# Performance work log

Hardware: AMD Instinct MI355X
Metric: run time of the kernel (lower is better)

Reference implementation:

```python
import jax, jax.numpy as jnp
import numpy as np

B, T, D, H = 4, 4096, 1280, 5120  # batch, tokens (64x64 SAM grid), embedding_dim, mlp_dim


def setup_inputs() -> dict:
    key = jax.random.key(0)
    k = jax.random.split(key, 5)
    # int8 quantized activations and weights (symmetric, per-tensor)
    x = jax.random.randint(k[0], (B, T, D), -128, 128, dtype=jnp.int8)
    w1 = jax.random.randint(k[1], (H, D), -128, 128, dtype=jnp.int8)  # lin1.weight [out,in]
    b1 = jax.random.normal(k[2], (H,), jnp.float32) * 0.02            # fp32 bias
    w2 = jax.random.randint(k[3], (D, H), -128, 128, dtype=jnp.int8)  # lin2.weight [out,in]
    b2 = jax.random.normal(k[4], (D,), jnp.float32) * 0.02
    a1 = jnp.float32(0.05 * 0.01)   # input_scale * w1_scale (dequant alpha of lin1)
    s_req = jnp.float32(0.08)       # lin2_input_scale (requant scale after GELU)
    a2 = jnp.float32(0.08 * 0.01)   # lin2_input_scale * w2_scale (dequant alpha of lin2)
    return dict(x=x, w1=w1, b1=b1, w2=w2, b2=b2, a1=a1, s_req=s_req, a2=a2)


def reference(x, w1, b1, w2, b2, a1, s_req, a2):
    acc1 = jnp.einsum('btd,hd->bth', x.astype(jnp.int32), w1.astype(jnp.int32))
    h = acc1.astype(jnp.float32) * a1 + b1              # [B,T,H] fp32
    # exact (erf) GELU, then requantize to int8 for lin2's input
    g = jax.nn.gelu(h, approximate=False)
    q = jnp.clip(jnp.round(g / s_req), -128, 127).astype(jnp.int8)
    acc2 = jnp.einsum('bth,dh->btd', q.astype(jnp.int32), w2.astype(jnp.int32))
    return acc2.astype(jnp.float32) * a2 + b2           # [B,T,D] fp32
```

## Files before the change

kernel.cpp:

```cpp
#include <hip/hip_runtime.h>
#include <stdint.h>
#include <math.h>

typedef __attribute__((ext_vector_type(4))) int i32x4;
typedef __attribute__((ext_vector_type(4))) float f32x4;

constexpr int D_DIM = 1280;
constexpr int H_DIM = 5120;

__device__ __forceinline__ void gload_lds16(const void* g, void* l) {
  __builtin_amdgcn_global_load_lds(
      (const __attribute__((address_space(1))) void*)g,
      (__attribute__((address_space(3))) void*)l,
      16, 0, 0);
}

__device__ __forceinline__ float gelu_fast(float h) {
  const float x = h * 0.70710678118f;
  const float ax = fabsf(x);
  const float t = __frcp_rn(__builtin_fmaf(0.3275911f, ax, 1.0f));
  float p = __builtin_fmaf(1.061405429f, t, -1.453152027f);
  p = __builtin_fmaf(p, t, 1.421413741f);
  p = __builtin_fmaf(p, t, -0.284496736f);
  p = __builtin_fmaf(p, t, 0.254829592f);
  p *= t;
  const float e = __expf(-x * x);
  const float erf_ax = __builtin_fmaf(-p, e, 1.0f);
  const float erf_x = copysignf(erf_ax, x);
  return 0.5f * h * (1.0f + erf_x);
}

__global__ void __launch_bounds__(256) k_packw(const int* __restrict__ s1,
                                               const int* __restrict__ s2,
                                               int8_t* __restrict__ out,
                                               long wn) {
  long i = ((long)blockIdx.x * 256 + threadIdx.x) * 16;
  const int* p = (i < wn) ? (s1 + i) : (s2 + (i - wn));
  i32x4 a = *(const i32x4*)(p);
  i32x4 b = *(const i32x4*)(p + 4);
  i32x4 c = *(const i32x4*)(p + 8);
  i32x4 d = *(const i32x4*)(p + 12);
  i32x4 r;
  r.x = (a.x & 255) | ((a.y & 255) << 8) | ((a.z & 255) << 16) | (a.w << 24);
  r.y = (b.x & 255) | ((b.y & 255) << 8) | ((b.z & 255) << 16) | (b.w << 24);
  r.z = (c.x & 255) | ((c.y & 255) << 8) | ((c.z & 255) << 16) | (c.w << 24);
  r.w = (d.x & 255) | ((d.y & 255) << 8) | ((d.z & 255) << 16) | (d.w << 24);
  *(i32x4*)(out + i) = r;
}

__global__ void __launch_bounds__(256) k_pack(const int* __restrict__ in,
                                              int8_t* __restrict__ out,
                                              long n) {
  long i = ((long)blockIdx.x * 256 + threadIdx.x) * 16;
  if (i >= n) return;
  const int* p = in + i;
  i32x4 a = *(const i32x4*)(p);
  i32x4 b = *(const i32x4*)(p + 4);
  i32x4 c = *(const i32x4*)(p + 8);
  i32x4 d = *(const i32x4*)(p + 12);
  i32x4 r;
  r.x = (a.x & 255) | ((a.y & 255) << 8) | ((a.z & 255) << 16) | (a.w << 24);
  r.y = (b.x & 255) | ((b.y & 255) << 8) | ((b.z & 255) << 16) | (b.w << 24);
  r.z = (c.x & 255) | ((c.y & 255) << 8) | ((c.z & 255) << 16) | (c.w << 24);
  r.w = (d.x & 255) | ((d.y & 255) << 8) | ((d.z & 255) << 16) | (d.w << 24);
  *(i32x4*)(out + i) = r;
}

template <int KDIM, int NDIM, bool GELU>
__global__ void __launch_bounds__(256, 2)
k_gemm(const int8_t* __restrict__ A, const int8_t* __restrict__ B,
       const float* __restrict__ bias, const float* __restrict__ ps1,
       const float* __restrict__ ps2, void* __restrict__ Cout, int Mtiles) {
  constexpr int BM = 128, BN = 128, BKB = 128;
  constexpr int NT = KDIM / BKB;
  constexpr int BNC = NDIM / BN;
  constexpr int G = BNC * 4;

  __shared__ __align__(16) int8_t As[2][BM * BKB];
  __shared__ __align__(16) int8_t Bs[2][BN * BKB];

  const int nwg = Mtiles * BNC;
  int bm, bn;
  {
    const int bid = blockIdx.x;
    const int q = nwg >> 3, r = nwg & 7, x = bid & 7, l = bid >> 3;
    const int swz = (x < r ? x * (q + 1) : r * (q + 1) + (x - r) * q) + l;
    if ((Mtiles & 3) == 0) {
      const int g = swz / G, rr = swz % G;
      bn = rr >> 2;
      bm = g * 4 + (rr & 3);
    } else {
      bn = swz % BNC;
      bm = swz / BNC;
    }
  }

  const int tid = threadIdx.x;
  const int lane = tid & 63, wid = tid >> 6;
  const int wr = wid >> 1, wc = wid & 1;

  const int srow = tid >> 3;
  const int soff = (((tid & 7) ^ (srow & 7)) << 4);
  const int8_t* Ath = A + (size_t)(bm * BM + srow) * KDIM + soff;
  const int8_t* Bth = B + (size_t)(bn * BN + srow) * KDIM + soff;
  const int dT = tid * 16;

  auto STAGE = [&](int buf, int t) {
    const int8_t* ga = Ath + t * BKB;
    const int8_t* gb = Bth + t * BKB;
#pragma unroll
    for (int p = 0; p < 4; ++p)
      gload_lds16(ga + (size_t)(p * 32) * KDIM, &As[buf][dT + p * 4096]);
#pragma unroll
    for (int p = 0; p < 4; ++p)
      gload_lds16(gb + (size_t)(p * 32) * KDIM, &Bs[buf][dT + p * 4096]);
  };

  const int r0 = lane & 15, kq = (lane >> 4) << 4;
  const int fsw = (r0 & 7) << 4;
  const int kof0 = kq ^ fsw;
  const int kof1 = (64 + kq) ^ fsw;
  const int rowA0 = (wr * 64 + r0) * BKB;
  const int rowB0 = (wc * 64 + r0) * BKB;

  i32x4 acc[4][4] = {};

  auto COMPUTE = [&](int buf) {
    const int8_t* Ac = As[buf];
    const int8_t* Bc = Bs[buf];
#pragma unroll
    for (int j = 0; j < 2; ++j) {
      const int kof = j ? kof1 : kof0;
      i32x4 af[4], bf[4];
#pragma unroll
      for (int m = 0; m < 4; ++m) af[m] = *(const i32x4*)(Ac + rowA0 + m * 2048 + kof);
#pragma unroll
      for (int n = 0; n < 4; ++n) bf[n] = *(const i32x4*)(Bc + rowB0 + n * 2048 + kof);
      if constexpr (GELU) {
#pragma unroll
        for (int n = 0; n < 4; ++n)
#pragma unroll
          for (int m = 0; m < 4; ++m)
            acc[n][m] =
                __builtin_amdgcn_mfma_i32_16x16x64_i8(bf[n], af[m], acc[n][m], 0, 0, 0);
      } else {
#pragma unroll
        for (int m = 0; m < 4; ++m)
#pragma unroll
          for (int n = 0; n < 4; ++n)
            acc[m][n] =
                __builtin_amdgcn_mfma_i32_16x16x64_i8(af[m], bf[n], acc[m][n], 0, 0, 0);
      }
    }
  };

  STAGE(0, 0);
  __syncthreads();
#pragma unroll 1
  for (int t = 0; t < NT; ++t) {
    const int cur = t & 1;
    if (t + 1 < NT) STAGE(cur ^ 1, t + 1);
    COMPUTE(cur);
    __syncthreads();
  }

  const int hq = lane >> 4;
  if constexpr (GELU) {
    const float s1 = *ps1;
    const float rs = 1.0f / (*ps2);
    int8_t* Q = (int8_t*)Cout;
    const int hb0 = bn * BN + wc * 64 + hq * 4;
    const int tok0 = bm * BM + wr * 64 + r0;
#pragma unroll
    for (int n = 0; n < 4; ++n) {
      const int hb = hb0 + n * 16;
      const f32x4 bv = *(const f32x4*)(bias + hb);
#pragma unroll
      for (int m = 0; m < 4; ++m) {
        const int tok = tok0 + m * 16;
        uint32_t pk = 0;
#pragma unroll
        for (int r = 0; r < 4; ++r) {
          const float h = __builtin_fmaf((float)acc[n][m][r], s1, bv[r]);
          float qf = rintf(gelu_fast(h) * rs);
          qf = fminf(127.0f, fmaxf(-128.0f, qf));
          pk |= ((uint32_t)((int)qf & 255)) << (r * 8);
        }
        *(uint32_t*)(Q + (size_t)tok * NDIM + hb) = pk;
      }
    }
  } else {
    const float s1 = *ps1;
    float* O = (float*)Cout;
    const int rowb = bm * BM + wr * 64 + hq * 4;
    const int colb = bn * BN + wc * 64 + r0;
#pragma unroll
    for (int n = 0; n < 4; ++n) {
      const int col = colb + n * 16;
      const float bv = bias[col];
#pragma unroll
      for (int m = 0; m < 4; ++m) {
#pragma unroll
        for (int r = 0; r < 4; ++r) {
          const int row = rowb + m * 16 + r;
          O[(size_t)row * NDIM + col] = __builtin_fmaf((float)acc[m][n][r], s1, bv);
        }
      }
    }
  }
}

extern "C" void kernel_launch(void* const* d_in, const int* in_sizes, int n_in,
                              void* d_out, int out_size, void* d_ws, size_t ws_size,
                              hipStream_t stream) {
  (void)in_sizes; (void)n_in; (void)out_size;
  const int*   x32  = (const int*)d_in[0];
  const int*   w132 = (const int*)d_in[1];
  const float* b1   = (const float*)d_in[2];
  const int*   w232 = (const int*)d_in[3];
  const float* b2   = (const float*)d_in[4];
  const float* a1   = (const float*)d_in[5];
  const float* sreq = (const float*)d_in[6];
  const float* a2   = (const float*)d_in[7];
  float* out = (float*)d_out;

  const int M = 4 * 4096;
  const size_t WN = (size_t)H_DIM * D_DIM;
  constexpr int BM = 128, BN = 128;

  int8_t* w1p  = (int8_t*)d_ws;
  int8_t* w2p  = w1p + WN;
  int8_t* base = w2p + WN;

  size_t avail = ws_size > 2 * WN ? ws_size - 2 * WN : 0;
  size_t rows = avail / (size_t)(D_DIM + H_DIM);
  int Mc = (int)((rows / BM) * BM);
  if (Mc > M) Mc = M;
  if (Mc < BM) Mc = BM;

  k_packw<<<(int)(2 * WN / 4096), 256, 0, stream>>>(w132, w232, w1p, (long)WN);

  for (int m0 = 0; m0 < M; m0 += Mc) {
    const int mc = (M - m0 < Mc) ? (M - m0) : Mc;
    int8_t* xp = base;
    int8_t* q  = base + (size_t)Mc * D_DIM;
    const size_t nx = (size_t)mc * D_DIM;
    const int mt = mc / BM;
    k_pack<<<(int)(nx / 4096), 256, 0, stream>>>(x32 + (size_t)m0 * D_DIM, xp, (long)nx);
    k_gemm<D_DIM, H_DIM, true><<<mt * (H_DIM / BN), 256, 0, stream>>>(
        xp, w1p, b1, a1, sreq, q, mt);
    k_gemm<H_DIM, D_DIM, false><<<mt * (D_DIM / BN), 256, 0, stream>>>(
        q, w2p, b2, a2, nullptr, out + (size_t)m0 * D_DIM, mt);
  }
}
```

Measured before the change: 333.4 us.

## Switch int8 GEMMs to 32x32x32 MFMA with LDS-staged coalesced GELU output

Replaces the 16x16x64 int8 MFMA tiling with 32x32x32 MFMA instructions, a 2x2 grid of 32x32 accumulators per wave, and fewer LDS fragment loads per k-step. The main loop is unrolled by two with a fixed double-buffer layout in one flat shared array and precomputed fragment pointers. The GELU epilogue now writes packed int8 results into swizzled LDS and then does coalesced 16-byte global stores instead of scattered 4-byte stores. This adds an extra barrier and LDS round trip in the epilogue, and the unrolled loop assumes an even number of k-tiles.

```diff
diff --git a/kernel.cpp b/kernel.cpp
--- a/kernel.cpp
+++ b/kernel.cpp
@@ -3,6 +3,7 @@
 #include <math.h>
 
 typedef __attribute__((ext_vector_type(4))) int i32x4;
+typedef __attribute__((ext_vector_type(16))) int i32x16;
 typedef __attribute__((ext_vector_type(4))) float f32x4;
 
 constexpr int D_DIM = 1280;
@@ -76,8 +77,7 @@
   constexpr int BNC = NDIM / BN;
   constexpr int G = BNC * 4;
 
-  __shared__ __align__(16) int8_t As[2][BM * BKB];
-  __shared__ __align__(16) int8_t Bs[2][BN * BKB];
+  __shared__ __align__(16) int8_t smem[4 * 16384];
 
   const int nwg = Mtiles * BNC;
   int bm, bn;
@@ -105,106 +105,121 @@
   const int8_t* Bth = B + (size_t)(bn * BN + srow) * KDIM + soff;
   const int dT = tid * 16;
 
-  auto STAGE = [&](int buf, int t) {
-    const int8_t* ga = Ath + t * BKB;
-    const int8_t* gb = Bth + t * BKB;
+  auto STAGE = [&](int boff, const int8_t* ga, const int8_t* gb) {
 #pragma unroll
     for (int p = 0; p < 4; ++p)
-      gload_lds16(ga + (size_t)(p * 32) * KDIM, &As[buf][dT + p * 4096]);
+      gload_lds16(ga + (size_t)(p * 32) * KDIM, smem + boff + dT + p * 4096);
 #pragma unroll
     for (int p = 0; p < 4; ++p)
-      gload_lds16(gb + (size_t)(p * 32) * KDIM, &Bs[buf][dT + p * 4096]);
+      gload_lds16(gb + (size_t)(p * 32) * KDIM,
+                  smem + 32768 + boff + dT + p * 4096);
   };
 
-  const int r0 = lane & 15, kq = (lane >> 4) << 4;
-  const int fsw = (r0 & 7) << 4;
-  const int kof0 = kq ^ fsw;
-  const int kof1 = (64 + kq) ^ fsw;
-  const int rowA0 = (wr * 64 + r0) * BKB;
-  const int rowB0 = (wc * 64 + r0) * BKB;
-
-  i32x4 acc[4][4] = {};
-
-  auto COMPUTE = [&](int buf) {
-    const int8_t* Ac = As[buf];
-    const int8_t* Bc = Bs[buf];
-#pragma unroll
-    for (int j = 0; j < 2; ++j) {
-      const int kof = j ? kof1 : kof0;
-      i32x4 af[4], bf[4];
-#pragma unroll
-      for (int m = 0; m < 4; ++m) af[m] = *(const i32x4*)(Ac + rowA0 + m * 2048 + kof);
-#pragma unroll
-      for (int n = 0; n < 4; ++n) bf[n] = *(const i32x4*)(Bc + rowB0 + n * 2048 + kof);
+  const int r32 = lane & 31, hi5 = lane >> 5;
+  const int fsw = (lane & 7) << 4;
+  const int kq = hi5 << 4;
+  const int8_t* aP[4];
+  const int8_t* bP[4];
+#pragma unroll
+  for (int ks = 0; ks < 4; ++ks) {
+    const int koff = (ks * 32 + kq) ^ fsw;
+    aP[ks] = smem + (wr * 64 + r32) * BKB + koff;
+    bP[ks] = smem + 32768 + (wc * 64 + r32) * BKB + koff;
+  }
+
+  i32x16 acc[2][2] = {};
+
+  auto COMPUTE = [&](int boff) {
+#pragma unroll
+    for (int ks = 0; ks < 4; ++ks) {
+      i32x4 a0 = *(const i32x4*)(aP[ks] + boff);
+      i32x4 a1 = *(const i32x4*)(aP[ks] + boff + 4096);
+      i32x4 b0 = *(const i32x4*)(bP[ks] + boff);
+      i32x4 b1 = *(const i32x4*)(bP[ks] + boff + 4096);
       if constexpr (GELU) {
-#pragma unroll
-        for (int n = 0; n < 4; ++n)
-#pragma unroll
-          for (int m = 0; m < 4; ++m)
-            acc[n][m] =
-                __builtin_amdgcn_mfma_i32_16x16x64_i8(bf[n], af[m], acc[n][m], 0, 0, 0);
+        acc[0][0] = __builtin_amdgcn_mfma_i32_32x32x32_i8(b0, a0, acc[0][0], 0, 0, 0);
+        acc[0][1] = __builtin_amdgcn_mfma_i32_32x32x32_i8(b0, a1, acc[0][1], 0, 0, 0);
+        acc[1][0] = __builtin_amdgcn_mfma_i32_32x32x32_i8(b1, a0, acc[1][0], 0, 0, 0);
+        acc[1][1] = __builtin_amdgcn_mfma_i32_32x32x32_i8(b1, a1, acc[1][1], 0, 0, 0);
       } else {
-#pragma unroll
-        for (int m = 0; m < 4; ++m)
-#pragma unroll
-          for (int n = 0; n < 4; ++n)
-            acc[m][n] =
-                __builtin_amdgcn_mfma_i32_16x16x64_i8(af[m], bf[n], acc[m][n], 0, 0, 0);
+        acc[0][0] = __builtin_amdgcn_mfma_i32_32x32x32_i8(a0, b0, acc[0][0], 0, 0, 0);
+        acc[0][1] = __builtin_amdgcn_mfma_i32_32x32x32_i8(a0, b1, acc[0][1], 0, 0, 0);
+        acc[1][0] = __builtin_amdgcn_mfma_i32_32x32x32_i8(a1, b0, acc[1][0], 0, 0, 0);
+        acc[1][1] = __builtin_amdgcn_mfma_i32_32x32x32_i8(a1, b1, acc[1][1], 0, 0, 0);
       }
     }
   };
 
-  STAGE(0, 0);
+  STAGE(0, Ath, Bth);
   __syncthreads();
+  const int8_t* gA = Ath + BKB;
+  const int8_t* gB = Bth + BKB;
 #pragma unroll 1
-  for (int t = 0; t < NT; ++t) {
-    const int cur = t & 1;
-    if (t + 1 < NT) STAGE(cur ^ 1, t + 1);
-    COMPUTE(cur);
+  for (int t = 0; t < NT; t += 2) {
+    STAGE(16384, gA, gB);
+    COMPUTE(0);
     __syncthreads();
-  }
-
-  const int hq = lane >> 4;
+    if (t + 2 < NT) STAGE(0, gA + BKB, gB + BKB);
+    COMPUTE(16384);
+    __syncthreads();
+    gA += 2 * BKB;
+    gB += 2 * BKB;
+  }
+
   if constexpr (GELU) {
     const float s1 = *ps1;
     const float rs = 1.0f / (*ps2);
     int8_t* Q = (int8_t*)Cout;
-    const int hb0 = bn * BN + wc * 64 + hq * 4;
-    const int tok0 = bm * BM + wr * 64 + r0;
-#pragma unroll
-    for (int n = 0; n < 4; ++n) {
-      const int hb = hb0 + n * 16;
-      const f32x4 bv = *(const f32x4*)(bias + hb);
-#pragma unroll
-      for (int m = 0; m < 4; ++m) {
-        const int tok = tok0 + m * 16;
-        uint32_t pk = 0;
-#pragma unroll
-        for (int r = 0; r < 4; ++r) {
-          const float h = __builtin_fmaf((float)acc[n][m][r], s1, bv[r]);
-          float qf = rintf(gelu_fast(h) * rs);
-          qf = fminf(127.0f, fmaxf(-128.0f, qf));
-          pk |= ((uint32_t)((int)qf & 255)) << (r * 8);
+    int8_t* lb = smem;
+#pragma unroll
+    for (int n = 0; n < 2; ++n) {
+#pragma unroll
+      for (int q = 0; q < 4; ++q) {
+        const int hl = wc * 64 + n * 32 + q * 8 + hi5 * 4;
+        const f32x4 bv = *(const f32x4*)(bias + bn * BN + hl);
+#pragma unroll
+        for (int m = 0; m < 2; ++m) {
+          uint32_t pk = 0;
+#pragma unroll
+          for (int rr = 0; rr < 4; ++rr) {
+            const float h = __builtin_fmaf((float)acc[n][m][q * 4 + rr], s1, bv[rr]);
+            float qf = rintf(gelu_fast(h) * rs);
+            qf = fminf(127.0f, fmaxf(-128.0f, qf));
+            pk |= ((uint32_t)((int)qf & 255)) << (rr * 8);
+          }
+          const int row = wr * 64 + m * 32 + r32;
+          const int ad = row * 128 + ((((hl >> 4) ^ (row & 7)) << 4)) + (hl & 12);
+          *(uint32_t*)(lb + ad) = pk;
         }
-        *(uint32_t*)(Q + (size_t)tok * NDIM + hb) = pk;
       }
+    }
+    __syncthreads();
+#pragma unroll
+    for (int it = 0; it < 4; ++it) {
+      const int row = wid * 32 + it * 8 + (lane >> 3);
+      const int sl = lane & 7;
+      i32x4 v = *(const i32x4*)(lb + row * 128 + ((sl ^ (row & 7)) << 4));
+      *(i32x4*)(Q + (size_t)(bm * BM + row) * NDIM + bn * BN + sl * 16) = v;
     }
   } else {
     const float s1 = *ps1;
     float* O = (float*)Cout;
-    const int rowb = bm * BM + wr * 64 + hq * 4;
-    const int colb = bn * BN + wc * 64 + r0;
-#pragma unroll
-    for (int n = 0; n < 4; ++n) {
-      const int col = colb + n * 16;
+    const int colb = bn * BN + wc * 64 + r32;
+#pragma unroll
+    for (int n = 0; n < 2; ++n) {
+      const int col = colb + n * 32;
       const float bv = bias[col];
 #pragma unroll
-      for (int m = 0; m < 4; ++m) {
-#pragma unroll
-        for (int r = 0; r < 4; ++r) {
-          const int row = rowb + m * 16 + r;
-          O[(size_t)row * NDIM + col] = __builtin_fmaf((float)acc[m][n][r], s1, bv);
-        }
+      for (int m = 0; m < 2; ++m) {
+        const int rowb = bm * BM + wr * 64 + m * 32 + hi5 * 4;
+#pragma unroll
+        for (int q = 0; q < 4; ++q)
+#pragma unroll
+          for (int rr = 0; rr < 4; ++rr) {
+            const int row = rowb + q * 8 + rr;
+            O[(size_t)row * NDIM + col] =
+                __builtin_fmaf((float)acc[m][n][q * 4 + rr], s1, bv);
+          }
       }
     }
   }
```

Result: faster. 314.9 us (-5.6%).
